# Kernel tuning notes

Measured on AMD Instinct MI355X. Metric: run time of the kernel, lower is better.

Reference implementation:

```python
import jax, jax.numpy as jnp
import numpy as np
import math

B, T, C, H = 2, 4096, 512, 8
HD = C // H


def setup_inputs() -> dict:
    key = jax.random.key(0)
    k1, k2, k3 = jax.random.split(key, 3)
    x = jax.random.normal(k1, (B, T, C), dtype=jnp.float32)
    # weights stored as [in, out] so y = x @ W (equivalent to torch Linear with W^T)
    w_qkv = jax.random.normal(k2, (C, 3 * C), dtype=jnp.float32) * (1.0 / math.sqrt(C))
    w_out = jax.random.normal(k3, (C, C), dtype=jnp.float32) * (1.0 / math.sqrt(C))
    return {"x": x, "w_qkv": w_qkv, "w_out": w_out}


def reference(x, w_qkv, w_out):
    Bs, Ts, Cs = x.shape
    qkv = x @ w_qkv                                   # [B,T,3C]
    q, k, v = jnp.split(qkv, 3, axis=-1)
    # [B,H,T,HD]
    q = q.reshape(Bs, Ts, H, HD).transpose(0, 2, 1, 3)
    k = k.reshape(Bs, Ts, H, HD).transpose(0, 2, 1, 3)
    v = v.reshape(Bs, Ts, H, HD).transpose(0, 2, 1, 3)
    scores = jnp.einsum("bhqd,bhkd->bhqk", q, k) / math.sqrt(HD)
    causal = jnp.tril(jnp.ones((Ts, Ts), dtype=bool))
    scores = jnp.where(causal[None, None], scores, -jnp.inf)
    attn = jax.nn.softmax(scores, axis=-1)            # [B,H,T,T]
    out = jnp.einsum("bhqk,bhkd->bhqd", attn, v)      # [B,H,T,HD]
    out = out.transpose(0, 2, 1, 3).reshape(Bs, Ts, Cs)
    return out @ w_out
```

## Files before the change

kernel.cpp:

```cpp
#include <hip/hip_runtime.h>
#include <hip/hip_bf16.h>

typedef __bf16 bf16;
typedef __bf16 bf16x4 __attribute__((ext_vector_type(4)));
typedef __bf16 bf16x8 __attribute__((ext_vector_type(8)));
typedef float f32x4 __attribute__((ext_vector_type(4)));

#define BB 2
#define TT 4096
#define CC 512
#define HH 8
#define HD 64
#define BHD 16
#define M_TOT 8192

#define SCL (0.125f * 1.44269504f)

#if __has_builtin(__builtin_amdgcn_exp2f)
#define EXP2F(x) __builtin_amdgcn_exp2f(x)
#else
#define EXP2F(x) exp2f(x)
#endif

#define GLDS(gptr, lptr)                                                     \
  __builtin_amdgcn_global_load_lds(                                          \
      (const __attribute__((address_space(1))) void*)(gptr),                 \
      (__attribute__((address_space(3))) void*)(lptr), 16, 0, 0)

__global__ __launch_bounds__(256) void convert_x_kernel(
    const float* __restrict__ X, bf16* __restrict__ Xb) {
  const size_t i0 = ((size_t)blockIdx.x * 256 + threadIdx.x) * 16;
  const float4* p = (const float4*)(X + i0);
#pragma unroll
  for (int c = 0; c < 2; ++c) {
    float4 a = p[c * 2], b = p[c * 2 + 1];
    bf16x8 v;
    v[0] = (bf16)a.x; v[1] = (bf16)a.y; v[2] = (bf16)a.z; v[3] = (bf16)a.w;
    v[4] = (bf16)b.x; v[5] = (bf16)b.y; v[6] = (bf16)b.z; v[7] = (bf16)b.w;
    *(bf16x8*)&Xb[i0 + c * 8] = v;
  }
}

__global__ __launch_bounds__(256) void transpose_w_kernel(
    const float* __restrict__ Wq, const float* __restrict__ Wo,
    bf16* __restrict__ WQT, bf16* __restrict__ WOT) {
  __shared__ float tile[64][65];
  int b = blockIdx.x;
  const float* W; bf16* WT; int N, n0, k0;
  if (b < 192) { W = Wq; WT = WQT; N = 1536; n0 = (b % 24) * 64; k0 = (b / 24) * 64; }
  else { b -= 192; W = Wo; WT = WOT; N = 512; n0 = (b & 7) * 64; k0 = (b >> 3) * 64; }
  const int t = threadIdx.x;
  const int rr = t >> 4, cc4 = (t & 15) * 4;
#pragma unroll
  for (int i = 0; i < 4; ++i) {
    float4 v = *(const float4*)&W[(size_t)(k0 + rr + i * 16) * N + n0 + cc4];
    tile[rr + i * 16][cc4 + 0] = v.x;
    tile[rr + i * 16][cc4 + 1] = v.y;
    tile[rr + i * 16][cc4 + 2] = v.z;
    tile[rr + i * 16][cc4 + 3] = v.w;
  }
  __syncthreads();
#pragma unroll
  for (int i = 0; i < 4; ++i) {
    const int nn = rr + i * 16;
    bf16x4 o;
#pragma unroll
    for (int j = 0; j < 4; ++j) o[j] = (bf16)tile[cc4 + j][nn];
    *(bf16x4*)&WT[(size_t)(n0 + nn) * 512 + k0 + cc4] = o;
  }
}

__global__ __launch_bounds__(256) void gemm_qkv_kernel(
    const bf16* __restrict__ Xb, const bf16* __restrict__ Wt,
    bf16* __restrict__ qw, bf16* __restrict__ kw, bf16* __restrict__ vw) {
  __shared__ __align__(16) bf16 As[128 * 64];
  __shared__ __align__(16) bf16 Bs[128 * 64];
  const int tid = threadIdx.x;
  const int wid = tid >> 6, lane = tid & 63, ln = lane & 15, hi = lane >> 4;
  const int wr = wid >> 1, wc = wid & 1;
  const int m0 = blockIdx.x * 128, n0 = blockIdx.y * 128;
  const int srow = lane >> 3, srcc = (lane & 7) ^ srow;

  f32x4 acc[4][4] = {};

  for (int k0 = 0; k0 < 512; k0 += 64) {
    __syncthreads();
#pragma unroll
    for (int i = 0; i < 4; ++i) {
      const int rb = 32 * wid + 8 * i;
      GLDS(&Xb[(size_t)(m0 + rb + srow) * 512 + k0 + srcc * 8], &As[rb * 64]);
      GLDS(&Wt[(size_t)(n0 + rb + srow) * 512 + k0 + srcc * 8], &Bs[rb * 64]);
    }
    __syncthreads();

    bf16x8 af[4][2], bfr[4][2];
#pragma unroll
    for (int mi = 0; mi < 4; ++mi) {
      const int row = wr * 64 + mi * 16 + ln, rs = row & 7;
      af[mi][0] = *(const bf16x8*)&As[row * 64 + ((hi ^ rs) * 8)];
      af[mi][1] = *(const bf16x8*)&As[row * 64 + (((4 + hi) ^ rs) * 8)];
    }
#pragma unroll
    for (int ni = 0; ni < 4; ++ni) {
      const int row = wc * 64 + ni * 16 + ln, rs = row & 7;
      bfr[ni][0] = *(const bf16x8*)&Bs[row * 64 + ((hi ^ rs) * 8)];
      bfr[ni][1] = *(const bf16x8*)&Bs[row * 64 + (((4 + hi) ^ rs) * 8)];
    }
#pragma unroll
    for (int mi = 0; mi < 4; ++mi)
#pragma unroll
      for (int ni = 0; ni < 4; ++ni) {
        acc[mi][ni] = __builtin_amdgcn_mfma_f32_16x16x32_bf16(af[mi][0], bfr[ni][0], acc[mi][ni], 0, 0, 0);
        acc[mi][ni] = __builtin_amdgcn_mfma_f32_16x16x32_bf16(af[mi][1], bfr[ni][1], acc[mi][ni], 0, 0, 0);
      }
  }

#pragma unroll
  for (int mi = 0; mi < 4; ++mi) {
    int rowb = m0 + wr * 64 + mi * 16 + hi * 4;
    int b = rowb >> 12, t0 = rowb & 4095;
#pragma unroll
    for (int ni = 0; ni < 4; ++ni) {
      int n = n0 + wc * 64 + ni * 16 + ln;
      int which = n >> 9, c = n & 511, h = c >> 6, d = c & 63;
      if (which == 2) {
        bf16x4 pv;
#pragma unroll
        for (int r = 0; r < 4; ++r) pv[r] = (bf16)acc[mi][ni][r];
        *(bf16x4*)&vw[((size_t)(b * HH + h) * HD + d) * TT + t0] = pv;
      } else {
        bf16* dst = which ? kw : qw;
        const float sc = which ? 1.0f : SCL;
#pragma unroll
        for (int r = 0; r < 4; ++r)
          dst[((size_t)(b * HH + h) * TT + t0 + r) * HD + d] = (bf16)(acc[mi][ni][r] * sc);
      }
    }
  }
}

__global__ __launch_bounds__(256) void attn_piece_kernel(
    const bf16* __restrict__ qw, const bf16* __restrict__ kw,
    const bf16* __restrict__ vt,
    bf16* __restrict__ po, float* __restrict__ pl) {
  __shared__ __align__(16) bf16 Ks[2][64 * 64];
  __shared__ __align__(16) bf16 Vs[2][64 * 64];
  const int tid = threadIdx.x;
  const int wid = tid >> 6, lane = tid & 63, ln = lane & 15, hi = lane >> 4;

  int qb, bh, chunk;
  {
    const int pid = blockIdx.x;
    if (pid < 512)       { qb = 31 - (pid >> 6); int r = pid & 63; bh = r >> 2; chunk = r & 3; }
    else if (pid < 896)  { int l = pid - 512; qb = 23 - l / 48; int r = l % 48; bh = r / 3; chunk = r % 3; }
    else if (pid < 1152) { int l = pid - 896; qb = 15 - (l >> 5); int r = l & 31; bh = r >> 1; chunk = r & 1; }
    else                 { int l = pid - 1152; qb = 7 - (l >> 4); bh = l & 15; chunk = 0; }
  }
  const int t0c = chunk * 16;
  const int ntot = 2 * qb + 2;
  const int t1 = (t0c + 16 < ntot) ? (t0c + 16) : ntot;
  const int pid = blockIdx.x;

  const int q0w = qb * 128 + wid * 32;

  const int lrow8 = lane >> 3, lch = lane & 7;
  const int srcch = lch ^ lrow8;
  const int rbase = 8 * wid + lrow8;
  const size_t kb = (size_t)bh * TT * HD, vb = (size_t)bh * HD * TT;

  bf16x8 qf[2][2];
#pragma unroll
  for (int qi = 0; qi < 2; ++qi)
#pragma unroll
    for (int h = 0; h < 2; ++h)
      qf[qi][h] = *(const bf16x8*)&qw[((size_t)bh * TT + q0w + qi * 16 + ln) * HD + h * 32 + hi * 8];

  const bf16* kp[4][2];
#pragma unroll
  for (int kt = 0; kt < 4; ++kt) {
    const int krow = kt * 16 + ln;
    kp[kt][0] = &Ks[0][krow * 64 + ((hi ^ (ln & 7)) * 8)];
    kp[kt][1] = &Ks[0][krow * 64 + (((4 + hi) ^ (ln & 7)) * 8)];
  }
  const bf16* vp[4][2][2];
#pragma unroll
  for (int db = 0; db < 4; ++db) {
    const int d = db * 16 + ln, rowb = d * 64, dx = d & 7;
#pragma unroll
    for (int h2 = 0; h2 < 2; ++h2) {
      const int c1 = h2 * 4 + (hi >> 1);
      vp[db][h2][0] = &Vs[0][rowb + ((c1 ^ dx) * 8) + (hi & 1) * 4];
      vp[db][h2][1] = &Vs[0][rowb + (((c1 + 2) ^ dx) * 8) + (hi & 1) * 4];
    }
  }

  f32x4 o[2][4] = {};
  f32x4 osum[2] = {};

  bf16x8 vones;
#pragma unroll
  for (int j = 0; j < 8; ++j) vones[j] = (bf16)1.0f;

  {
    const int kv = t0c * 64;
    GLDS(kw + kb + (size_t)(kv + rbase) * HD + srcch * 8, &Ks[0][(8 * wid) * 64]);
    GLDS(kw + kb + (size_t)(kv + 32 + rbase) * HD + srcch * 8, &Ks[0][(32 + 8 * wid) * 64]);
    GLDS(vt + vb + (size_t)rbase * TT + kv + srcch * 8, &Vs[0][(8 * wid) * 64]);
    GLDS(vt + vb + (size_t)(32 + rbase) * TT + kv + srcch * 8, &Vs[0][(32 + 8 * wid) * 64]);
  }
  const bf16* pk0 = kw + kb + (size_t)((t0c + 1) * 64 + rbase) * HD + srcch * 8;
  const bf16* pk1 = pk0 + (size_t)32 * HD;
  const bf16* pv0 = vt + vb + (size_t)rbase * TT + (t0c + 1) * 64 + srcch * 8;
  const bf16* pv1 = pv0 + (size_t)32 * TT;
  __syncthreads();

#define TILE(t_, BUF) do {                                                   \
    const int kv0 = (t_) * 64;                                               \
    if ((t_) + 1 < t1) {                                                     \
      GLDS(pk0, &Ks[(BUF) ^ 1][(8 * wid) * 64]);                             \
      GLDS(pk1, &Ks[(BUF) ^ 1][(32 + 8 * wid) * 64]);                        \
      GLDS(pv0, &Vs[(BUF) ^ 1][(8 * wid) * 64]);                             \
      GLDS(pv1, &Vs[(BUF) ^ 1][(32 + 8 * wid) * 64]);                        \
      pk0 += (size_t)64 * HD; pk1 += (size_t)64 * HD; pv0 += 64; pv1 += 64;  \
    }                                                                        \
    if (kv0 <= q0w + 31) {                                                   \
      f32x4 s[2][4];                                                         \
      __builtin_amdgcn_s_setprio(1);                                         \
      _Pragma("unroll")                                                      \
      for (int kt = 0; kt < 4; ++kt) {                                       \
        bf16x8 kf0 = *(const bf16x8*)(kp[kt][0] + (BUF) * 4096);             \
        bf16x8 kf1 = *(const bf16x8*)(kp[kt][1] + (BUF) * 4096);             \
        _Pragma("unroll")                                                    \
        for (int qi = 0; qi < 2; ++qi) {                                     \
          f32x4 a = {};                                                      \
          a = __builtin_amdgcn_mfma_f32_16x16x32_bf16(kf0, qf[qi][0], a, 0, 0, 0); \
          a = __builtin_amdgcn_mfma_f32_16x16x32_bf16(kf1, qf[qi][1], a, 0, 0, 0); \
          s[qi][kt] = a;                                                     \
        }                                                                    \
      }                                                                      \
      __builtin_amdgcn_s_setprio(0);                                         \
      _Pragma("unroll")                                                      \
      for (int qi = 0; qi < 2; ++qi) {                                       \
        if (kv0 + 63 > q0w + qi * 16) {                                      \
          const int qg = q0w + qi * 16 + ln;                                 \
          _Pragma("unroll")                                                  \
          for (int kt = 0; kt < 4; ++kt)                                     \
            _Pragma("unroll")                                                \
            for (int r = 0; r < 4; ++r)                                      \
              if (kv0 + kt * 16 + hi * 4 + r > qg) s[qi][kt][r] = -1e30f;    \
        }                                                                    \
      }                                                                      \
      _Pragma("unroll")                                                      \
      for (int qi = 0; qi < 2; ++qi)                                         \
        _Pragma("unroll")                                                    \
        for (int kt = 0; kt < 4; ++kt)                                       \
          _Pragma("unroll")                                                  \
          for (int r = 0; r < 4; ++r) s[qi][kt][r] = EXP2F(s[qi][kt][r]);    \
      bf16x8 pa[2][2];                                                       \
      _Pragma("unroll")                                                      \
      for (int qi = 0; qi < 2; ++qi)                                         \
        _Pragma("unroll")                                                    \
        for (int h2 = 0; h2 < 2; ++h2)                                       \
          _Pragma("unroll")                                                  \
          for (int j = 0; j < 8; ++j)                                        \
            pa[qi][h2][j] = (bf16)s[qi][h2 * 2 + (j >> 2)][j & 3];           \
      __builtin_amdgcn_s_setprio(1);                                         \
      _Pragma("unroll")                                                      \
      for (int qi = 0; qi < 2; ++qi) {                                       \
        osum[qi] = __builtin_amdgcn_mfma_f32_16x16x32_bf16(pa[qi][0], vones, osum[qi], 0, 0, 0); \
        osum[qi] = __builtin_amdgcn_mfma_f32_16x16x32_bf16(pa[qi][1], vones, osum[qi], 0, 0, 0); \
      }                                                                      \
      _Pragma("unroll")                                                      \
      for (int db = 0; db < 4; ++db) {                                       \
        _Pragma("unroll")                                                    \
        for (int h2 = 0; h2 < 2; ++h2) {                                     \
          bf16x4 lo = *(const bf16x4*)(vp[db][h2][0] + (BUF) * 4096);        \
          bf16x4 hi4 = *(const bf16x4*)(vp[db][h2][1] + (BUF) * 4096);       \
          bf16x8 vf = __builtin_shufflevector(lo, hi4, 0, 1, 2, 3, 4, 5, 6, 7); \
          _Pragma("unroll")                                                  \
          for (int qi = 0; qi < 2; ++qi)                                     \
            o[qi][db] = __builtin_amdgcn_mfma_f32_16x16x32_bf16(pa[qi][h2], vf, o[qi][db], 0, 0, 0); \
        }                                                                    \
      }                                                                      \
      __builtin_amdgcn_s_setprio(0);                                         \
    }                                                                        \
    __syncthreads();                                                         \
  } while (0)

  int t = t0c;
  for (; t + 1 < t1; t += 2) { TILE(t, 0); TILE(t + 1, 1); }
  if (t < t1) TILE(t, 0);

  {
    bf16* ob = po + (size_t)pid * 8192;
#pragma unroll
    for (int qi = 0; qi < 2; ++qi)
#pragma unroll
      for (int db = 0; db < 4; ++db)
#pragma unroll
        for (int r = 0; r < 4; ++r)
          ob[(wid * 32 + qi * 16 + hi * 4 + r) * 64 + db * 16 + ln] = (bf16)o[qi][db][r];
    if (ln == 0) {
#pragma unroll
      for (int qi = 0; qi < 2; ++qi)
#pragma unroll
        for (int r = 0; r < 4; ++r)
          pl[pid * 128 + wid * 32 + qi * 16 + hi * 4 + r] = osum[qi][r];
    }
  }
#undef TILE
}

__global__ __launch_bounds__(256) void attn_combine_kernel(
    const bf16* __restrict__ po, const float* __restrict__ pl,
    bf16* __restrict__ aw) {
  const int cb = blockIdx.x;
  const int qb = 31 - (cb >> 4), bh = cb & 15;
  const int tid = threadIdx.x;
  const int q_ = tid >> 1, dc = (tid & 1) * 32;

  int nch, p0;
  if (qb >= 24)      { nch = 4; p0 = (31 - qb) * 64 + bh * 4; }
  else if (qb >= 16) { nch = 3; p0 = 512 + (23 - qb) * 48 + bh * 3; }
  else if (qb >= 8)  { nch = 2; p0 = 896 + (15 - qb) * 32 + bh * 2; }
  else               { nch = 1; p0 = 1152 + (7 - qb) * 16 + bh; }

  float sum = 0.f;
  for (int c = 0; c < nch; ++c) sum += pl[(p0 + c) * 128 + q_];
  const float inv = 1.0f / sum;

  float acc[32] = {};
  for (int c = 0; c < nch; ++c) {
    const bf16* ob = po + (size_t)(p0 + c) * 8192 + q_ * 64 + dc;
#pragma unroll
    for (int cc = 0; cc < 4; ++cc) {
      bf16x8 x = *(const bf16x8*)&ob[cc * 8];
#pragma unroll
      for (int j = 0; j < 8; ++j) acc[cc * 8 + j] += (float)x[j];
    }
  }
  bf16* dst = aw + ((size_t)bh * TT + qb * 128 + q_) * 64 + dc;
#pragma unroll
  for (int cc = 0; cc < 4; ++cc) {
    bf16x8 outv;
#pragma unroll
    for (int j = 0; j < 8; ++j) outv[j] = (bf16)(acc[cc * 8 + j] * inv);
    *(bf16x8*)&dst[cc * 8] = outv;
  }
}

__global__ __launch_bounds__(256) void gemm_out_kernel(
    const bf16* __restrict__ A, const bf16* __restrict__ Wot,
    float* __restrict__ out) {
  __shared__ __align__(16) bf16 As[128 * 64];
  __shared__ __align__(16) bf16 Bs[64 * 64];
  const int tid = threadIdx.x;
  const int wid = tid >> 6, lane = tid & 63, ln = lane & 15, hi = lane >> 4;
  const int wr = wid >> 1, wc = wid & 1;
  const int m0 = blockIdx.x * 128, n0 = blockIdx.y * 64;
  const int srow = lane >> 3, srcc = (lane & 7) ^ srow;

  f32x4 acc[4][2] = {};

  for (int k0 = 0; k0 < 512; k0 += 64) {
    const int h = k0 >> 6;
    __syncthreads();
#pragma unroll
    for (int i = 0; i < 4; ++i) {
      const int rb = 32 * wid + 8 * i;
      const int m = m0 + rb + srow;
      const int b = m >> 12, t = m & 4095;
      GLDS(&A[((size_t)(b * HH + h) * TT + t) * HD + srcc * 8], &As[rb * 64]);
    }
#pragma unroll
    for (int i = 0; i < 2; ++i) {
      const int rb = 16 * wid + 8 * i;
      GLDS(&Wot[(size_t)(n0 + rb + srow) * 512 + k0 + srcc * 8], &Bs[rb * 64]);
    }
    __syncthreads();

    bf16x8 af[4][2], bfr[2][2];
#pragma unroll
    for (int mi = 0; mi < 4; ++mi) {
      const int row = wr * 64 + mi * 16 + ln, rs = row & 7;
      af[mi][0] = *(const bf16x8*)&As[row * 64 + ((hi ^ rs) * 8)];
      af[mi][1] = *(const bf16x8*)&As[row * 64 + (((4 + hi) ^ rs) * 8)];
    }
#pragma unroll
    for (int ni = 0; ni < 2; ++ni) {
      const int row = wc * 32 + ni * 16 + ln, rs = row & 7;
      bfr[ni][0] = *(const bf16x8*)&Bs[row * 64 + ((hi ^ rs) * 8)];
      bfr[ni][1] = *(const bf16x8*)&Bs[row * 64 + (((4 + hi) ^ rs) * 8)];
    }
#pragma unroll
    for (int mi = 0; mi < 4; ++mi)
#pragma unroll
      for (int ni = 0; ni < 2; ++ni) {
        acc[mi][ni] = __builtin_amdgcn_mfma_f32_16x16x32_bf16(af[mi][0], bfr[ni][0], acc[mi][ni], 0, 0, 0);
        acc[mi][ni] = __builtin_amdgcn_mfma_f32_16x16x32_bf16(af[mi][1], bfr[ni][1], acc[mi][ni], 0, 0, 0);
      }
  }

#pragma unroll
  for (int mi = 0; mi < 4; ++mi) {
    int rowb = m0 + wr * 64 + mi * 16 + hi * 4;
#pragma unroll
    for (int ni = 0; ni < 2; ++ni) {
      int n = n0 + wc * 32 + ni * 16 + ln;
#pragma unroll
      for (int r = 0; r < 4; ++r)
        out[(size_t)(rowb + r) * 512 + n] = acc[mi][ni][r];
    }
  }
}

extern "C" void kernel_launch(void* const* d_in, const int* in_sizes, int n_in,
                              void* d_out, int out_size, void* d_ws, size_t ws_size,
                              hipStream_t stream) {
  const float* x = (const float*)d_in[0];
  const float* w_qkv = (const float*)d_in[1];
  const float* w_out = (const float*)d_in[2];
  float* out = (float*)d_out;

  const size_t QKV_ELEMS = (size_t)BHD * TT * HD;
  bf16* qw = (bf16*)d_ws;
  bf16* kw = qw + QKV_ELEMS;
  bf16* vw = kw + QKV_ELEMS;
  bf16* aw = vw + QKV_ELEMS;
  bf16* po = aw + QKV_ELEMS;
  float* pl = (float*)(po + (size_t)1280 * 8192);
  bf16* wqt = (bf16*)(pl + (size_t)1280 * 128);
  bf16* wot = wqt + (size_t)1536 * 512;
  bf16* xb = po;

  convert_x_kernel<<<1024, 256, 0, stream>>>(x, xb);
  transpose_w_kernel<<<256, 256, 0, stream>>>(w_qkv, w_out, wqt, wot);
  gemm_qkv_kernel<<<dim3(M_TOT / 128, 1536 / 128), 256, 0, stream>>>(xb, wqt, qw, kw, vw);
  attn_piece_kernel<<<1280, 256, 0, stream>>>(qw, kw, vw, po, pl);
  attn_combine_kernel<<<512, 256, 0, stream>>>(po, pl, aw);
  gemm_out_kernel<<<dim3(M_TOT / 128, 512 / 64), 256, 0, stream>>>(aw, wot, out);
}
```

Measured before the change: 121.8 us.

## Use 8 waves per block with 16 query rows each and finer KV chunks

Attention blocks grow from 256 to 512 threads. Each of the 8 waves now owns 16 query rows instead of 32, so a block still covers 128 queries. Each wave loads one 8-row slice of the K/V tile. KV splits shrink from 16 tiles to 8 tiles per chunk, raising the grid from 1280 to 2304 pieces, and the combine kernel's piece mapping and the workspace offsets change to match. The aim is more parallelism, better occupancy and latency hiding, and a less skewed causal tail. The costs are more partial outputs to write and combine, and less reuse of each K/V fragment across queries.

```diff
diff --git a/kernel.cpp b/kernel.cpp
--- a/kernel.cpp
+++ b/kernel.cpp
@@ -139,7 +139,7 @@
   }
 }
 
-__global__ __launch_bounds__(256) void attn_piece_kernel(
+__global__ __launch_bounds__(512, 8) void attn_piece_kernel(
     const bf16* __restrict__ qw, const bf16* __restrict__ kw,
     const bf16* __restrict__ vt,
     bf16* __restrict__ po, float* __restrict__ pl) {
@@ -148,32 +148,37 @@
   const int tid = threadIdx.x;
   const int wid = tid >> 6, lane = tid & 63, ln = lane & 15, hi = lane >> 4;
 
-  int qb, bh, chunk;
+  int qb2, bh, chunk;
   {
     const int pid = blockIdx.x;
-    if (pid < 512)       { qb = 31 - (pid >> 6); int r = pid & 63; bh = r >> 2; chunk = r & 3; }
-    else if (pid < 896)  { int l = pid - 512; qb = 23 - l / 48; int r = l % 48; bh = r / 3; chunk = r % 3; }
-    else if (pid < 1152) { int l = pid - 896; qb = 15 - (l >> 5); int r = l & 31; bh = r >> 1; chunk = r & 1; }
-    else                 { int l = pid - 1152; qb = 7 - (l >> 4); bh = l & 15; chunk = 0; }
-  }
-  const int t0c = chunk * 16;
-  const int ntot = 2 * qb + 2;
-  const int t1 = (t0c + 16 < ntot) ? (t0c + 16) : ntot;
+#define MAPB(OFF, K) { const int l = pid - (OFF);                            \
+      qb2 = (4 * (K) - 1) - l / (16 * (K));                                  \
+      const int r = l % (16 * (K)); bh = r / (K); chunk = r % (K); }
+    if      (pid < 512)  MAPB(0, 8)
+    else if (pid < 960)  MAPB(512, 7)
+    else if (pid < 1344) MAPB(960, 6)
+    else if (pid < 1664) MAPB(1344, 5)
+    else if (pid < 1920) MAPB(1664, 4)
+    else if (pid < 2112) MAPB(1920, 3)
+    else if (pid < 2240) MAPB(2112, 2)
+    else                 MAPB(2240, 1)
+#undef MAPB
+  }
+  const int ntot = 2 * qb2 + 2;
+  const int t0c = chunk * 8;
+  const int t1 = (t0c + 8 < ntot) ? (t0c + 8) : ntot;
   const int pid = blockIdx.x;
 
-  const int q0w = qb * 128 + wid * 32;
-
-  const int lrow8 = lane >> 3, lch = lane & 7;
-  const int srcch = lch ^ lrow8;
-  const int rbase = 8 * wid + lrow8;
+  const int q0w = qb2 * 128 + wid * 16;
+
+  const int rbase = 8 * wid + (lane >> 3);
+  const int srcch = (lane & 7) ^ (lane >> 3);
   const size_t kb = (size_t)bh * TT * HD, vb = (size_t)bh * HD * TT;
 
-  bf16x8 qf[2][2];
-#pragma unroll
-  for (int qi = 0; qi < 2; ++qi)
-#pragma unroll
-    for (int h = 0; h < 2; ++h)
-      qf[qi][h] = *(const bf16x8*)&qw[((size_t)bh * TT + q0w + qi * 16 + ln) * HD + h * 32 + hi * 8];
+  bf16x8 qf[2];
+#pragma unroll
+  for (int h = 0; h < 2; ++h)
+    qf[h] = *(const bf16x8*)&qw[((size_t)bh * TT + q0w + ln) * HD + h * 32 + hi * 8];
 
   const bf16* kp[4][2];
 #pragma unroll
@@ -194,8 +199,8 @@
     }
   }
 
-  f32x4 o[2][4] = {};
-  f32x4 osum[2] = {};
+  f32x4 o[4] = {};
+  f32x4 osum = {};
 
   bf16x8 vones;
 #pragma unroll
@@ -204,72 +209,53 @@
   {
     const int kv = t0c * 64;
     GLDS(kw + kb + (size_t)(kv + rbase) * HD + srcch * 8, &Ks[0][(8 * wid) * 64]);
-    GLDS(kw + kb + (size_t)(kv + 32 + rbase) * HD + srcch * 8, &Ks[0][(32 + 8 * wid) * 64]);
     GLDS(vt + vb + (size_t)rbase * TT + kv + srcch * 8, &Vs[0][(8 * wid) * 64]);
-    GLDS(vt + vb + (size_t)(32 + rbase) * TT + kv + srcch * 8, &Vs[0][(32 + 8 * wid) * 64]);
   }
   const bf16* pk0 = kw + kb + (size_t)((t0c + 1) * 64 + rbase) * HD + srcch * 8;
-  const bf16* pk1 = pk0 + (size_t)32 * HD;
   const bf16* pv0 = vt + vb + (size_t)rbase * TT + (t0c + 1) * 64 + srcch * 8;
-  const bf16* pv1 = pv0 + (size_t)32 * TT;
   __syncthreads();
 
 #define TILE(t_, BUF) do {                                                   \
     const int kv0 = (t_) * 64;                                               \
     if ((t_) + 1 < t1) {                                                     \
       GLDS(pk0, &Ks[(BUF) ^ 1][(8 * wid) * 64]);                             \
-      GLDS(pk1, &Ks[(BUF) ^ 1][(32 + 8 * wid) * 64]);                        \
       GLDS(pv0, &Vs[(BUF) ^ 1][(8 * wid) * 64]);                             \
-      GLDS(pv1, &Vs[(BUF) ^ 1][(32 + 8 * wid) * 64]);                        \
-      pk0 += (size_t)64 * HD; pk1 += (size_t)64 * HD; pv0 += 64; pv1 += 64;  \
+      pk0 += (size_t)64 * HD; pv0 += 64;                                     \
     }                                                                        \
-    if (kv0 <= q0w + 31) {                                                   \
-      f32x4 s[2][4];                                                         \
+    if (kv0 <= q0w + 15) {                                                   \
+      f32x4 s[4];                                                            \
       __builtin_amdgcn_s_setprio(1);                                         \
       _Pragma("unroll")                                                      \
       for (int kt = 0; kt < 4; ++kt) {                                       \
         bf16x8 kf0 = *(const bf16x8*)(kp[kt][0] + (BUF) * 4096);             \
         bf16x8 kf1 = *(const bf16x8*)(kp[kt][1] + (BUF) * 4096);             \
-        _Pragma("unroll")                                                    \
-        for (int qi = 0; qi < 2; ++qi) {                                     \
-          f32x4 a = {};                                                      \
-          a = __builtin_amdgcn_mfma_f32_16x16x32_bf16(kf0, qf[qi][0], a, 0, 0, 0); \
-          a = __builtin_amdgcn_mfma_f32_16x16x32_bf16(kf1, qf[qi][1], a, 0, 0, 0); \
-          s[qi][kt] = a;                                                     \
-        }                                                                    \
+        f32x4 a = {};                                                        \
+        a = __builtin_amdgcn_mfma_f32_16x16x32_bf16(kf0, qf[0], a, 0, 0, 0); \
+        a = __builtin_amdgcn_mfma_f32_16x16x32_bf16(kf1, qf[1], a, 0, 0, 0); \
+        s[kt] = a;                                                           \
       }                                                                      \
       __builtin_amdgcn_s_setprio(0);                                         \
-      _Pragma("unroll")                                                      \
-      for (int qi = 0; qi < 2; ++qi) {                                       \
-        if (kv0 + 63 > q0w + qi * 16) {                                      \
-          const int qg = q0w + qi * 16 + ln;                                 \
-          _Pragma("unroll")                                                  \
-          for (int kt = 0; kt < 4; ++kt)                                     \
-            _Pragma("unroll")                                                \
-            for (int r = 0; r < 4; ++r)                                      \
-              if (kv0 + kt * 16 + hi * 4 + r > qg) s[qi][kt][r] = -1e30f;    \
-        }                                                                    \
-      }                                                                      \
-      _Pragma("unroll")                                                      \
-      for (int qi = 0; qi < 2; ++qi)                                         \
+      if (kv0 + 63 > q0w) {                                                  \
+        const int qg = q0w + ln;                                             \
         _Pragma("unroll")                                                    \
         for (int kt = 0; kt < 4; ++kt)                                       \
           _Pragma("unroll")                                                  \
-          for (int r = 0; r < 4; ++r) s[qi][kt][r] = EXP2F(s[qi][kt][r]);    \
-      bf16x8 pa[2][2];                                                       \
+          for (int r = 0; r < 4; ++r)                                        \
+            if (kv0 + kt * 16 + hi * 4 + r > qg) s[kt][r] = -1e30f;          \
+      }                                                                      \
       _Pragma("unroll")                                                      \
-      for (int qi = 0; qi < 2; ++qi)                                         \
+      for (int kt = 0; kt < 4; ++kt)                                         \
         _Pragma("unroll")                                                    \
-        for (int h2 = 0; h2 < 2; ++h2)                                       \
-          _Pragma("unroll")                                                  \
-          for (int j = 0; j < 8; ++j)                                        \
-            pa[qi][h2][j] = (bf16)s[qi][h2 * 2 + (j >> 2)][j & 3];           \
+        for (int r = 0; r < 4; ++r) s[kt][r] = EXP2F(s[kt][r]);              \
+      bf16x8 pa[2];                                                          \
+      _Pragma("unroll")                                                      \
+      for (int h2 = 0; h2 < 2; ++h2)                                         \
+        _Pragma("unroll")                                                    \
+        for (int j = 0; j < 8; ++j)                                          \
+          pa[h2][j] = (bf16)s[h2 * 2 + (j >> 2)][j & 3];                     \
       __builtin_amdgcn_s_setprio(1);                                         \
-      _Pragma("unroll")                                                      \
-      for (int qi = 0; qi < 2; ++qi) {                                       \
-        osum[qi] = __builtin_amdgcn_mfma_f32_16x16x32_bf16(pa[qi][0], vones, osum[qi], 0, 0, 0); \
-        osum[qi] = __builtin_amdgcn_mfma_f32_16x16x32_bf16(pa[qi][1], vones, osum[qi], 0, 0, 0); \
-      }                                                                      \
+      osum = __builtin_amdgcn_mfma_f32_16x16x32_bf16(pa[0], vones, osum, 0, 0, 0); \
+      osum = __builtin_amdgcn_mfma_f32_16x16x32_bf16(pa[1], vones, osum, 0, 0, 0); \
       _Pragma("unroll")                                                      \
       for (int db = 0; db < 4; ++db) {                                       \
         _Pragma("unroll")                                                    \
@@ -277,9 +263,7 @@
           bf16x4 lo = *(const bf16x4*)(vp[db][h2][0] + (BUF) * 4096);        \
           bf16x4 hi4 = *(const bf16x4*)(vp[db][h2][1] + (BUF) * 4096);       \
           bf16x8 vf = __builtin_shufflevector(lo, hi4, 0, 1, 2, 3, 4, 5, 6, 7); \
-          _Pragma("unroll")                                                  \
-          for (int qi = 0; qi < 2; ++qi)                                     \
-            o[qi][db] = __builtin_amdgcn_mfma_f32_16x16x32_bf16(pa[qi][h2], vf, o[qi][db], 0, 0, 0); \
+          o[db] = __builtin_amdgcn_mfma_f32_16x16x32_bf16(pa[h2], vf, o[db], 0, 0, 0); \
         }                                                                    \
       }                                                                      \
       __builtin_amdgcn_s_setprio(0);                                         \
@@ -294,18 +278,14 @@
   {
     bf16* ob = po + (size_t)pid * 8192;
 #pragma unroll
-    for (int qi = 0; qi < 2; ++qi)
-#pragma unroll
-      for (int db = 0; db < 4; ++db)
-#pragma unroll
-        for (int r = 0; r < 4; ++r)
-          ob[(wid * 32 + qi * 16 + hi * 4 + r) * 64 + db * 16 + ln] = (bf16)o[qi][db][r];
+    for (int db = 0; db < 4; ++db)
+#pragma unroll
+      for (int r = 0; r < 4; ++r)
+        ob[(wid * 16 + hi * 4 + r) * 64 + db * 16 + ln] = (bf16)o[db][r];
     if (ln == 0) {
 #pragma unroll
-      for (int qi = 0; qi < 2; ++qi)
-#pragma unroll
-        for (int r = 0; r < 4; ++r)
-          pl[pid * 128 + wid * 32 + qi * 16 + hi * 4 + r] = osum[qi][r];
+      for (int r = 0; r < 4; ++r)
+        pl[pid * 128 + wid * 16 + hi * 4 + r] = osum[r];
     }
   }
 #undef TILE
@@ -315,22 +295,20 @@
     const bf16* __restrict__ po, const float* __restrict__ pl,
     bf16* __restrict__ aw) {
   const int cb = blockIdx.x;
-  const int qb = 31 - (cb >> 4), bh = cb & 15;
+  const int qb2 = 31 - (cb >> 4), bh = cb & 15;
   const int tid = threadIdx.x;
   const int q_ = tid >> 1, dc = (tid & 1) * 32;
 
-  int nch, p0;
-  if (qb >= 24)      { nch = 4; p0 = (31 - qb) * 64 + bh * 4; }
-  else if (qb >= 16) { nch = 3; p0 = 512 + (23 - qb) * 48 + bh * 3; }
-  else if (qb >= 8)  { nch = 2; p0 = 896 + (15 - qb) * 32 + bh * 2; }
-  else               { nch = 1; p0 = 1152 + (7 - qb) * 16 + bh; }
+  const int k = (qb2 >> 2) + 1;
+  static const int OFF[9] = {0, 2240, 2112, 1920, 1664, 1344, 960, 512, 0};
+  const int p0 = OFF[k] + ((4 * k - 1) - qb2) * 16 * k + bh * k;
 
   float sum = 0.f;
-  for (int c = 0; c < nch; ++c) sum += pl[(p0 + c) * 128 + q_];
+  for (int c = 0; c < k; ++c) sum += pl[(p0 + c) * 128 + q_];
   const float inv = 1.0f / sum;
 
   float acc[32] = {};
-  for (int c = 0; c < nch; ++c) {
+  for (int c = 0; c < k; ++c) {
     const bf16* ob = po + (size_t)(p0 + c) * 8192 + q_ * 64 + dc;
 #pragma unroll
     for (int cc = 0; cc < 4; ++cc) {
@@ -339,7 +317,7 @@
       for (int j = 0; j < 8; ++j) acc[cc * 8 + j] += (float)x[j];
     }
   }
-  bf16* dst = aw + ((size_t)bh * TT + qb * 128 + q_) * 64 + dc;
+  bf16* dst = aw + ((size_t)bh * TT + qb2 * 128 + q_) * 64 + dc;
 #pragma unroll
   for (int cc = 0; cc < 4; ++cc) {
     bf16x8 outv;
@@ -428,15 +406,15 @@
   bf16* vw = kw + QKV_ELEMS;
   bf16* aw = vw + QKV_ELEMS;
   bf16* po = aw + QKV_ELEMS;
-  float* pl = (float*)(po + (size_t)1280 * 8192);
-  bf16* wqt = (bf16*)(pl + (size_t)1280 * 128);
+  float* pl = (float*)(po + (size_t)2304 * 8192);
+  bf16* wqt = (bf16*)(pl + (size_t)2304 * 128);
   bf16* wot = wqt + (size_t)1536 * 512;
   bf16* xb = po;
 
   convert_x_kernel<<<1024, 256, 0, stream>>>(x, xb);
   transpose_w_kernel<<<256, 256, 0, stream>>>(w_qkv, w_out, wqt, wot);
   gemm_qkv_kernel<<<dim3(M_TOT / 128, 1536 / 128), 256, 0, stream>>>(xb, wqt, qw, kw, vw);
-  attn_piece_kernel<<<1280, 256, 0, stream>>>(qw, kw, vw, po, pl);
+  attn_piece_kernel<<<2304, 512, 0, stream>>>(qw, kw, vw, po, pl);
   attn_combine_kernel<<<512, 256, 0, stream>>>(po, pl, aw);
   gemm_out_kernel<<<dim3(M_TOT / 128, 512 / 64), 256, 0, stream>>>(aw, wot, out);
 }
```

Result: slower. 153.8 us (+26.3%).

## Use 256-query attention blocks with 8 waves and pre-permuted V layout

Applied to the files above, without the earlier changes.

The attention piece kernel now uses 512-thread blocks covering 256 queries, so each K/V tile loaded into shared memory serves twice as many queries. The split-KV chunk size drops to 8 tiles, and the block-to-work map and the combine kernel are rebuilt to match. The QKV GEMM writes V with a permuted token order inside each 64-token group, so the PV stage can read each B fragment with one 16-byte LDS load instead of two 8-byte loads plus a shuffle. In exchange there are fewer blocks, more threads per block and added register pressure under the (512,4) launch bounds.

```diff
diff --git a/kernel.cpp b/kernel.cpp
--- a/kernel.cpp
+++ b/kernel.cpp
@@ -127,7 +127,10 @@
         bf16x4 pv;
 #pragma unroll
         for (int r = 0; r < 4; ++r) pv[r] = (bf16)acc[mi][ni][r];
-        *(bf16x4*)&vw[((size_t)(b * HH + h) * HD + d) * TT + t0] = pv;
+        const int tb = t0 & 63;
+        const int paddr = (((tb >> 4) & 1) << 2) | (((tb >> 2) & 3) << 3) |
+                          ((tb >> 5) << 5);
+        *(bf16x4*)&vw[((size_t)(b * HH + h) * HD + d) * TT + (t0 & ~63) + paddr] = pv;
       } else {
         bf16* dst = which ? kw : qw;
         const float sc = which ? 1.0f : SCL;
@@ -139,7 +142,7 @@
   }
 }
 
-__global__ __launch_bounds__(256) void attn_piece_kernel(
+__global__ __launch_bounds__(512, 4) void attn_piece_kernel(
     const bf16* __restrict__ qw, const bf16* __restrict__ kw,
     const bf16* __restrict__ vt,
     bf16* __restrict__ po, float* __restrict__ pl) {
@@ -148,24 +151,31 @@
   const int tid = threadIdx.x;
   const int wid = tid >> 6, lane = tid & 63, ln = lane & 15, hi = lane >> 4;
 
-  int qb, bh, chunk;
+  int qb4, bh, chunk;
   {
     const int pid = blockIdx.x;
-    if (pid < 512)       { qb = 31 - (pid >> 6); int r = pid & 63; bh = r >> 2; chunk = r & 3; }
-    else if (pid < 896)  { int l = pid - 512; qb = 23 - l / 48; int r = l % 48; bh = r / 3; chunk = r % 3; }
-    else if (pid < 1152) { int l = pid - 896; qb = 15 - (l >> 5); int r = l & 31; bh = r >> 1; chunk = r & 1; }
-    else                 { int l = pid - 1152; qb = 7 - (l >> 4); bh = l & 15; chunk = 0; }
-  }
-  const int t0c = chunk * 16;
-  const int ntot = 2 * qb + 2;
-  const int t1 = (t0c + 16 < ntot) ? (t0c + 16) : ntot;
+#define MAPB(OFF, K) { const int l = pid - (OFF);                            \
+      qb4 = (2 * (K) - 1) - l / (16 * (K));                                  \
+      const int r = l % (16 * (K)); bh = r / (K); chunk = r % (K); }
+    if      (pid < 256)  MAPB(0, 8)
+    else if (pid < 480)  MAPB(256, 7)
+    else if (pid < 672)  MAPB(480, 6)
+    else if (pid < 832)  MAPB(672, 5)
+    else if (pid < 960)  MAPB(832, 4)
+    else if (pid < 1056) MAPB(960, 3)
+    else if (pid < 1120) MAPB(1056, 2)
+    else                 MAPB(1120, 1)
+#undef MAPB
+  }
+  const int ntot = 4 * qb4 + 4;
+  const int t0c = chunk * 8;
+  const int t1 = (t0c + 8 < ntot) ? (t0c + 8) : ntot;
   const int pid = blockIdx.x;
 
-  const int q0w = qb * 128 + wid * 32;
-
-  const int lrow8 = lane >> 3, lch = lane & 7;
-  const int srcch = lch ^ lrow8;
-  const int rbase = 8 * wid + lrow8;
+  const int q0w = qb4 * 256 + wid * 32;
+
+  const int rbase = 8 * wid + (lane >> 3);
+  const int srcch = (lane & 7) ^ (lane >> 3);
   const size_t kb = (size_t)bh * TT * HD, vb = (size_t)bh * HD * TT;
 
   bf16x8 qf[2][2];
@@ -182,16 +192,13 @@
     kp[kt][0] = &Ks[0][krow * 64 + ((hi ^ (ln & 7)) * 8)];
     kp[kt][1] = &Ks[0][krow * 64 + (((4 + hi) ^ (ln & 7)) * 8)];
   }
-  const bf16* vp[4][2][2];
+  const bf16* vp[4][2];
 #pragma unroll
   for (int db = 0; db < 4; ++db) {
     const int d = db * 16 + ln, rowb = d * 64, dx = d & 7;
 #pragma unroll
-    for (int h2 = 0; h2 < 2; ++h2) {
-      const int c1 = h2 * 4 + (hi >> 1);
-      vp[db][h2][0] = &Vs[0][rowb + ((c1 ^ dx) * 8) + (hi & 1) * 4];
-      vp[db][h2][1] = &Vs[0][rowb + (((c1 + 2) ^ dx) * 8) + (hi & 1) * 4];
-    }
+    for (int h2 = 0; h2 < 2; ++h2)
+      vp[db][h2] = &Vs[0][rowb + (((4 * h2 + hi) ^ dx) * 8)];
   }
 
   f32x4 o[2][4] = {};
@@ -204,24 +211,18 @@
   {
     const int kv = t0c * 64;
     GLDS(kw + kb + (size_t)(kv + rbase) * HD + srcch * 8, &Ks[0][(8 * wid) * 64]);
-    GLDS(kw + kb + (size_t)(kv + 32 + rbase) * HD + srcch * 8, &Ks[0][(32 + 8 * wid) * 64]);
     GLDS(vt + vb + (size_t)rbase * TT + kv + srcch * 8, &Vs[0][(8 * wid) * 64]);
-    GLDS(vt + vb + (size_t)(32 + rbase) * TT + kv + srcch * 8, &Vs[0][(32 + 8 * wid) * 64]);
   }
   const bf16* pk0 = kw + kb + (size_t)((t0c + 1) * 64 + rbase) * HD + srcch * 8;
-  const bf16* pk1 = pk0 + (size_t)32 * HD;
   const bf16* pv0 = vt + vb + (size_t)rbase * TT + (t0c + 1) * 64 + srcch * 8;
-  const bf16* pv1 = pv0 + (size_t)32 * TT;
   __syncthreads();
 
 #define TILE(t_, BUF) do {                                                   \
     const int kv0 = (t_) * 64;                                               \
     if ((t_) + 1 < t1) {                                                     \
       GLDS(pk0, &Ks[(BUF) ^ 1][(8 * wid) * 64]);                             \
-      GLDS(pk1, &Ks[(BUF) ^ 1][(32 + 8 * wid) * 64]);                        \
       GLDS(pv0, &Vs[(BUF) ^ 1][(8 * wid) * 64]);                             \
-      GLDS(pv1, &Vs[(BUF) ^ 1][(32 + 8 * wid) * 64]);                        \
-      pk0 += (size_t)64 * HD; pk1 += (size_t)64 * HD; pv0 += 64; pv1 += 64;  \
+      pk0 += (size_t)64 * HD; pv0 += 64;                                     \
     }                                                                        \
     if (kv0 <= q0w + 31) {                                                   \
       f32x4 s[2][4];                                                         \
@@ -274,9 +275,7 @@
       for (int db = 0; db < 4; ++db) {                                       \
         _Pragma("unroll")                                                    \
         for (int h2 = 0; h2 < 2; ++h2) {                                     \
-          bf16x4 lo = *(const bf16x4*)(vp[db][h2][0] + (BUF) * 4096);        \
-          bf16x4 hi4 = *(const bf16x4*)(vp[db][h2][1] + (BUF) * 4096);       \
-          bf16x8 vf = __builtin_shufflevector(lo, hi4, 0, 1, 2, 3, 4, 5, 6, 7); \
+          bf16x8 vf = *(const bf16x8*)(vp[db][h2] + (BUF) * 4096);           \
           _Pragma("unroll")                                                  \
           for (int qi = 0; qi < 2; ++qi)                                     \
             o[qi][db] = __builtin_amdgcn_mfma_f32_16x16x32_bf16(pa[qi][h2], vf, o[qi][db], 0, 0, 0); \
@@ -292,7 +291,7 @@
   if (t < t1) TILE(t, 0);
 
   {
-    bf16* ob = po + (size_t)pid * 8192;
+    bf16* ob = po + (size_t)pid * 16384;
 #pragma unroll
     for (int qi = 0; qi < 2; ++qi)
 #pragma unroll
@@ -305,7 +304,7 @@
       for (int qi = 0; qi < 2; ++qi)
 #pragma unroll
         for (int r = 0; r < 4; ++r)
-          pl[pid * 128 + wid * 32 + qi * 16 + hi * 4 + r] = osum[qi][r];
+          pl[pid * 256 + wid * 32 + qi * 16 + hi * 4 + r] = osum[qi][r];
     }
   }
 #undef TILE
@@ -315,23 +314,23 @@
     const bf16* __restrict__ po, const float* __restrict__ pl,
     bf16* __restrict__ aw) {
   const int cb = blockIdx.x;
-  const int qb = 31 - (cb >> 4), bh = cb & 15;
+  const int qb4 = 15 - (cb >> 5);
+  const int r5 = cb & 31;
+  const int bh = r5 >> 1, half = r5 & 1;
   const int tid = threadIdx.x;
-  const int q_ = tid >> 1, dc = (tid & 1) * 32;
-
-  int nch, p0;
-  if (qb >= 24)      { nch = 4; p0 = (31 - qb) * 64 + bh * 4; }
-  else if (qb >= 16) { nch = 3; p0 = 512 + (23 - qb) * 48 + bh * 3; }
-  else if (qb >= 8)  { nch = 2; p0 = 896 + (15 - qb) * 32 + bh * 2; }
-  else               { nch = 1; p0 = 1152 + (7 - qb) * 16 + bh; }
+  const int q_ = half * 128 + (tid >> 1), dc = (tid & 1) * 32;
+
+  const int k = (qb4 + 2) >> 1;
+  static const int OFF[9] = {0, 1120, 1056, 960, 832, 672, 480, 256, 0};
+  const int p0 = OFF[k] + ((2 * k - 1) - qb4) * 16 * k + bh * k;
 
   float sum = 0.f;
-  for (int c = 0; c < nch; ++c) sum += pl[(p0 + c) * 128 + q_];
+  for (int c = 0; c < k; ++c) sum += pl[(p0 + c) * 256 + q_];
   const float inv = 1.0f / sum;
 
   float acc[32] = {};
-  for (int c = 0; c < nch; ++c) {
-    const bf16* ob = po + (size_t)(p0 + c) * 8192 + q_ * 64 + dc;
+  for (int c = 0; c < k; ++c) {
+    const bf16* ob = po + (size_t)(p0 + c) * 16384 + q_ * 64 + dc;
 #pragma unroll
     for (int cc = 0; cc < 4; ++cc) {
       bf16x8 x = *(const bf16x8*)&ob[cc * 8];
@@ -339,7 +338,7 @@
       for (int j = 0; j < 8; ++j) acc[cc * 8 + j] += (float)x[j];
     }
   }
-  bf16* dst = aw + ((size_t)bh * TT + qb * 128 + q_) * 64 + dc;
+  bf16* dst = aw + ((size_t)bh * TT + qb4 * 256 + q_) * 64 + dc;
 #pragma unroll
   for (int cc = 0; cc < 4; ++cc) {
     bf16x8 outv;
@@ -428,15 +427,15 @@
   bf16* vw = kw + QKV_ELEMS;
   bf16* aw = vw + QKV_ELEMS;
   bf16* po = aw + QKV_ELEMS;
-  float* pl = (float*)(po + (size_t)1280 * 8192);
-  bf16* wqt = (bf16*)(pl + (size_t)1280 * 128);
+  float* pl = (float*)(po + (size_t)1152 * 16384);
+  bf16* wqt = (bf16*)(pl + (size_t)1152 * 256);
   bf16* wot = wqt + (size_t)1536 * 512;
   bf16* xb = po;
 
   convert_x_kernel<<<1024, 256, 0, stream>>>(x, xb);
   transpose_w_kernel<<<256, 256, 0, stream>>>(w_qkv, w_out, wqt, wot);
   gemm_qkv_kernel<<<dim3(M_TOT / 128, 1536 / 128), 256, 0, stream>>>(xb, wqt, qw, kw, vw);
-  attn_piece_kernel<<<1280, 256, 0, stream>>>(qw, kw, vw, po, pl);
+  attn_piece_kernel<<<1152, 512, 0, stream>>>(qw, kw, vw, po, pl);
   attn_combine_kernel<<<512, 256, 0, stream>>>(po, pl, aw);
   gemm_out_kernel<<<dim3(M_TOT / 128, 512 / 64), 256, 0, stream>>>(aw, wot, out);
 }
```

New measurement: 111.6 us. 8.3% less time.
